# Optimization experiments

Hardware: AMD Instinct MI355X
Metric: run time of the kernel (lower is better)

The kernel has to match this reference:

```python
import jax, jax.numpy as jnp
import numpy as np

B, S, N = 65536, 512, 514
EPS = 1e-16


def setup_inputs() -> dict:
    key = jax.random.key(0)
    kx, kv = jax.random.split(key)
    x = jax.random.normal(kx, (B, S), dtype=jnp.float32)
    # parameters: uniform(-1,1) then normalized along the size dim (as in reset_parameters)
    v = jax.random.uniform(kv, (N, S, 1), dtype=jnp.float32, minval=-1.0, maxval=1.0)
    v = v / jnp.linalg.norm(v, axis=1, keepdims=True)
    return {"x": x, "vectors": v}


def _calculate_Q(vectors):
    # vectors: [N, S, 1]
    Nv, Sv, _ = vectors.shape
    v = vectors[..., 0]                                   # [N, S]
    inner = jnp.sum(v * v, axis=1)[:, None, None]         # [N, 1, 1]  (v^T v)
    outer = v[:, :, None] * v[:, None, :]                 # [N, S, S]  (v v^T)
    I = jnp.eye(Sv, dtype=vectors.dtype)
    mats = I[None, :, :] - 2.0 * outer / (inner + EPS)    # [N, S, S]

    def step(Q, M):
        return Q @ M, None

    Q, _ = jax.lax.scan(step, mats[0], mats[1:])          # sequential product M0 @ M1 @ ... @ M_{N-1}
    return Q


def reference(x, vectors):
    Q = _calculate_Q(vectors)
    return x @ Q.T
```

## Files before the change

### kernel.cpp

```cpp
#include <hip/hip_runtime.h>


#define LDG 520
#define GROWS 528
#define LDU 520
#define NHH 514
#define SDIM 512
#define EPS_HH 1e-16f
#define EPLD 132

typedef float f32x4 __attribute__((ext_vector_type(4)));
typedef __fp16 h16x2 __attribute__((ext_vector_type(2)));
typedef __fp16 h16x8 __attribute__((ext_vector_type(8)));

__device__ __forceinline__ void gl_lds16(const void* g, void* l) {
  __builtin_amdgcn_global_load_lds((const __attribute__((address_space(1))) void*)g,
                                   (__attribute__((address_space(3))) void*)l, 16, 0, 0);
}

__global__ __launch_bounds__(256) void gram_k(const float* __restrict__ v,
                                              float* __restrict__ G) {
  __shared__ float As[32][36];
  __shared__ float Bs[32][36];
  const int t = threadIdx.x;
  const int i0 = blockIdx.y * 32, j0 = blockIdx.x * 32;
  const int tx = t & 15, ty = t >> 4;
  const int r = t >> 3, c4 = (t & 7) * 4;
  float acc00 = 0.f, acc01 = 0.f, acc10 = 0.f, acc11 = 0.f;
  for (int kb = 0; kb < SDIM; kb += 32) {
    __syncthreads();
    float4 av = (i0 + r < NHH)
                    ? *(const float4*)(v + (size_t)(i0 + r) * SDIM + kb + c4)
                    : make_float4(0.f, 0.f, 0.f, 0.f);
    float4 bv = (j0 + r < NHH)
                    ? *(const float4*)(v + (size_t)(j0 + r) * SDIM + kb + c4)
                    : make_float4(0.f, 0.f, 0.f, 0.f);
    *(float4*)&As[r][c4] = av;
    *(float4*)&Bs[r][c4] = bv;
    __syncthreads();
#pragma unroll
    for (int kk = 0; kk < 32; kk++) {
      float a0 = As[ty * 2][kk], a1 = As[ty * 2 + 1][kk];
      float b0 = Bs[tx * 2][kk], b1 = Bs[tx * 2 + 1][kk];
      acc00 = fmaf(a0, b0, acc00);
      acc01 = fmaf(a0, b1, acc01);
      acc10 = fmaf(a1, b0, acc10);
      acc11 = fmaf(a1, b1, acc11);
    }
  }
  int row0 = i0 + ty * 2, col0 = j0 + tx * 2;
  if (row0 < NHH) {
    if (col0 < LDG) G[(size_t)row0 * LDG + col0] = acc00;
    if (col0 + 1 < LDG) G[(size_t)row0 * LDG + col0 + 1] = acc01;
  }
  if (row0 + 1 < NHH) {
    if (col0 < LDG) G[(size_t)(row0 + 1) * LDG + col0] = acc10;
    if (col0 + 1 < LDG) G[(size_t)(row0 + 1) * LDG + col0 + 1] = acc11;
  }
}

__global__ __launch_bounds__(256, 1) void solve_k(const float* __restrict__ v,
                                                  const float* __restrict__ G,
                                                  float* __restrict__ U) {
  const int lane = threadIdx.x & 63;
  const int s = blockIdx.x * 4 + (threadIdx.x >> 6);
  float W[9];
  float binv[9];
#pragma unroll
  for (int k = 0; k < 9; k++) {
    int j = k * 64 + lane;
    W[k] = (j < NHH) ? v[(size_t)j * SDIM + s] : 0.f;
    binv[k] = (j < NHH) ? (2.0f / (G[(size_t)j * LDG + j] + EPS_HH)) : 0.f;
  }
  float* Urow = U + (size_t)s * LDU;
  float g[8][9];
#pragma unroll
  for (int p = 0; p < 7; p++) {
    const float* gp = G + (size_t)p * LDG + lane;
#pragma unroll
    for (int k = 0; k < 9; k++) g[p][k] = gp[k * 64];
  }
  float usave = 0.f;

#define HH_STEP(I, CI, SLOT, PSLOT, DO_PF)                                 \
  do {                                                                     \
    const int i_ = (I);                                                    \
    if (DO_PF) {                                                           \
      const float* gp_ = G + (size_t)(i_ + 7) * LDG + lane;                \
      _Pragma("unroll") for (int k = 0; k < 9; k++) g[PSLOT][k] =          \
          gp_[k * 64];                                                     \
    }                                                                      \
    const int sl_ = i_ & 63;                                               \
    float u_ = __shfl(W[CI] * binv[CI], sl_, 64);                          \
    if (lane == sl_) usave = u_;                                           \
    _Pragma("unroll") for (int k = 0; k < 9; k++) W[k] =                   \
        fmaf(-u_, g[SLOT][k], W[k]);                                       \
    if (sl_ == 63) Urow[i_ - 63 + lane] = usave;                           \
  } while (0)

#pragma unroll
  for (int c = 0; c < 8; c++) {
    for (int q = 0; q < 8; q++) {
      const int base = c * 64 + q * 8;
      HH_STEP(base + 0, c, 0, 7, true);
      HH_STEP(base + 1, c, 1, 0, true);
      HH_STEP(base + 2, c, 2, 1, true);
      HH_STEP(base + 3, c, 3, 2, true);
      HH_STEP(base + 4, c, 4, 3, true);
      HH_STEP(base + 5, c, 5, 4, true);
      HH_STEP(base + 6, c, 6, 5, true);
      HH_STEP(base + 7, c, 7, 6, true);
    }
  }
  HH_STEP(512, 8, 0, 0, false);
  HH_STEP(513, 8, 1, 0, false);
  if (lane < 2) Urow[512 + lane] = usave;
#undef HH_STEP
}

__global__ __launch_bounds__(256) void qtt_k(const float* __restrict__ v,
                                             const float* __restrict__ U,
                                             __fp16* __restrict__ QTT) {
  __shared__ float As[32][36];
  __shared__ float Bs[32][36];
  const int t = threadIdx.x;
  const int s0 = blockIdx.y * 32, t0 = blockIdx.x * 32;
  const int tx = t & 15, ty = t >> 4;
  const int r = t >> 3, c4 = (t & 7) * 4;
  float acc00 = 0.f, acc01 = 0.f, acc10 = 0.f, acc11 = 0.f;
  for (int kb = 0; kb < NHH; kb += 32) {
    __syncthreads();
    float4 av = *(const float4*)(U + (size_t)(s0 + r) * LDU + kb + c4);
    float4 bv = (kb + r < NHH)
                    ? *(const float4*)(v + (size_t)(kb + r) * SDIM + t0 + c4)
                    : make_float4(0.f, 0.f, 0.f, 0.f);
    *(float4*)&As[r][c4] = av;
    *(float4*)&Bs[r][c4] = bv;
    __syncthreads();
#pragma unroll
    for (int kk = 0; kk < 32; kk++) {
      float a0 = As[ty * 2][kk], a1 = As[ty * 2 + 1][kk];
      float b0 = Bs[kk][tx * 2], b1 = Bs[kk][tx * 2 + 1];
      acc00 = fmaf(a0, b0, acc00);
      acc01 = fmaf(a0, b1, acc01);
      acc10 = fmaf(a1, b0, acc10);
      acc11 = fmaf(a1, b1, acc11);
    }
  }
  int row0 = s0 + ty * 2, col0 = t0 + tx * 2;
  QTT[(size_t)row0 * SDIM + col0] =
      (__fp16)(((row0 == col0) ? 1.f : 0.f) - acc00);
  QTT[(size_t)row0 * SDIM + col0 + 1] =
      (__fp16)(((row0 == col0 + 1) ? 1.f : 0.f) - acc01);
  QTT[(size_t)(row0 + 1) * SDIM + col0] =
      (__fp16)(((row0 + 1 == col0) ? 1.f : 0.f) - acc10);
  QTT[(size_t)(row0 + 1) * SDIM + col0 + 1] =
      (__fp16)(((row0 + 1 == col0 + 1) ? 1.f : 0.f) - acc11);
}

__global__ __launch_bounds__(256) void gemm_k(const float* __restrict__ X,
                                              const __fp16* __restrict__ BT,
                                              float* __restrict__ C) {
  __shared__ __attribute__((aligned(16))) float As[2][128 * 32];
  __shared__ __attribute__((aligned(16))) __fp16 Bs[2][128 * 32];
  const int t = threadIdx.x;
  const int lane = t & 63, wave = t >> 6;
  const int bid = blockIdx.x;
  const int xcd = bid & 7;
  const int g = bid >> 3;
  const int m0 = ((g >> 2) * 8 + xcd) * 128;
  const int n0 = (g & 3) * 128;
  const int wm = (wave >> 1) * 64, wn = (wave & 1) * 64;
  const int rr = lane & 15, kg = lane >> 4;
  const int wb = t & ~63;

  f32x4 acc[4][4];
#pragma unroll
  for (int a = 0; a < 4; a++)
#pragma unroll
    for (int b = 0; b < 4; b++) acc[a][b] = (f32x4){0.f, 0.f, 0.f, 0.f};

  auto STAGE = [&](int k0, int buf) {
#pragma unroll
    for (int q = 0; q < 4; q++) {
      int idx = q * 256 + t;
      int r = idx >> 3, u = idx & 7;
      int c = (u ^ (r & 7)) * 4;
      const float* gp = X + (size_t)(m0 + r) * 512 + k0 + c;
      gl_lds16(gp, (void*)&As[buf][(size_t)(q * 256 + wb) * 4]);
    }
#pragma unroll
    for (int q = 0; q < 2; q++) {
      int idx = q * 256 + t;
      int r = idx >> 2, u = idx & 3;
      int c = (u ^ (r & 3)) * 8;
      const __fp16* gp = BT + (size_t)(n0 + r) * 512 + k0 + c;
      gl_lds16(gp, (void*)&Bs[buf][(size_t)(q * 256 + wb) * 8]);
    }
  };

  STAGE(0, 0);

  const int swzA = rr & 7;
  const int swzB = rr & 3;

  for (int ks = 0; ks < 16; ++ks) {
    const int cur = ks & 1;
    if (ks < 15) {
      STAGE((ks + 1) * 32, cur ^ 1);
      asm volatile("s_waitcnt vmcnt(6)" ::: "memory");
    } else {
      asm volatile("s_waitcnt vmcnt(0)" ::: "memory");
    }
    asm volatile("s_barrier" ::: "memory");

    h16x8 af[4], bf[4];
#pragma unroll
    for (int mi = 0; mi < 4; mi++) {
      const float* rowp = &As[cur][(size_t)(wm + mi * 16 + rr) * 32];
      float4 lo = *(const float4*)(rowp + (size_t)((2 * kg + 0) ^ swzA) * 4);
      float4 hi = *(const float4*)(rowp + (size_t)((2 * kg + 1) ^ swzA) * 4);
      h16x2 p0 = __builtin_amdgcn_cvt_pkrtz(lo.x, lo.y);
      h16x2 p1 = __builtin_amdgcn_cvt_pkrtz(lo.z, lo.w);
      h16x2 p2 = __builtin_amdgcn_cvt_pkrtz(hi.x, hi.y);
      h16x2 p3 = __builtin_amdgcn_cvt_pkrtz(hi.z, hi.w);
      h16x8 a = {p0[0], p0[1], p1[0], p1[1], p2[0], p2[1], p3[0], p3[1]};
      af[mi] = a;
    }
#pragma unroll
    for (int ni = 0; ni < 4; ni++) {
      const __fp16* rowp = &Bs[cur][(size_t)(wn + ni * 16 + rr) * 32];
      bf[ni] = *(const h16x8*)(rowp + (size_t)(kg ^ swzB) * 8);
    }

#pragma unroll
    for (int mi = 0; mi < 4; mi++)
#pragma unroll
      for (int ni = 0; ni < 4; ni++)
        acc[mi][ni] =
            __builtin_amdgcn_mfma_f32_16x16x32_f16(af[mi], bf[ni], acc[mi][ni], 0, 0, 0);

    asm volatile("s_barrier" ::: "memory");
  }

  float* Ep = (float*)As;
  const int lr = (lane >> 4) * 4;
  const int lc = wn + rr;
  const int buf = wave >> 1;
#pragma unroll
  for (int rnd = 0; rnd < 4; rnd++) {
    float* bp = Ep + buf * (16 * EPLD);
#pragma unroll
    for (int ni = 0; ni < 4; ni++)
#pragma unroll
      for (int q = 0; q < 4; q++)
        bp[(lr + q) * EPLD + lc + ni * 16] = acc[rnd][ni][q];
    __syncthreads();
#pragma unroll
    for (int j = 0; j < 4; j++) {
      int fidx = j * 256 + t;
      int b = fidx >> 9;
      int wi = fidx & 511;
      int lrow = wi >> 5;
      int c4 = wi & 31;
      int grow = m0 + b * 64 + rnd * 16 + lrow;
      *(float4*)(C + (size_t)grow * 512 + n0 + c4 * 4) =
          *(const float4*)(Ep + b * (16 * EPLD) + lrow * EPLD + c4 * 4);
    }
    __syncthreads();
  }
}

extern "C" void kernel_launch(void* const* d_in, const int* in_sizes, int n_in,
                              void* d_out, int out_size, void* d_ws, size_t ws_size,
                              hipStream_t stream) {
  const float* x = (const float*)d_in[0];
  const float* v = (const float*)d_in[1];
  float* out = (float*)d_out;

  char* w = (char*)d_ws;
  float* G = (float*)w;
  float* U = (float*)(w + (size_t)GROWS * LDG * 4);
  __fp16* QTT =
      (__fp16*)(w + (size_t)GROWS * LDG * 4 + (size_t)512 * LDU * 4);

  gram_k<<<dim3(17, 17), 256, 0, stream>>>(v, G);
  solve_k<<<128, 256, 0, stream>>>(v, G, U);
  qtt_k<<<dim3(16, 16), 256, 0, stream>>>(v, U, QTT);
  gemm_k<<<2048, 256, 0, stream>>>(x, QTT, out);
}
```

Baseline: 361.7 us.

## Enlarge gram/qtt tiles to 4x4 per thread and spread solve across more blocks

The gram and QTT matrix kernels move from 32x32 tiles with 2x2 outputs per thread to 64x64 tiles with 4x4 outputs per thread. K-major LDS layout allows float4 fragment reads, raising arithmetic intensity per LDS access and cutting the launched block count. The solve kernel now runs 2 waves per block across 256 blocks to spread rows over more CUs, and uses readlane instead of a shuffle for the broadcast. The QTT kernel pads K to 528 with clamped, zeroed loads and writes packed fp16x4 stores. Larger tiles give fewer blocks (81 and 64), which may underfill the GPU on these small matrices.

```diff
diff --git a/kernel.cpp b/kernel.cpp
--- a/kernel.cpp
+++ b/kernel.cpp
@@ -11,6 +11,7 @@
 
 typedef float f32x4 __attribute__((ext_vector_type(4)));
 typedef __fp16 h16x2 __attribute__((ext_vector_type(2)));
+typedef __fp16 h16x4v __attribute__((ext_vector_type(4)));
 typedef __fp16 h16x8 __attribute__((ext_vector_type(8)));
 
 __device__ __forceinline__ void gl_lds16(const void* g, void* l) {
@@ -20,50 +21,64 @@
 
 __global__ __launch_bounds__(256) void gram_k(const float* __restrict__ v,
                                               float* __restrict__ G) {
-  __shared__ float As[32][36];
-  __shared__ float Bs[32][36];
+  __shared__ float As[16][68];
+  __shared__ float Bs[16][68];
   const int t = threadIdx.x;
-  const int i0 = blockIdx.y * 32, j0 = blockIdx.x * 32;
+  const int i0 = blockIdx.y * 64, j0 = blockIdx.x * 64;
   const int tx = t & 15, ty = t >> 4;
-  const int r = t >> 3, c4 = (t & 7) * 4;
-  float acc00 = 0.f, acc01 = 0.f, acc10 = 0.f, acc11 = 0.f;
-  for (int kb = 0; kb < SDIM; kb += 32) {
-    __syncthreads();
-    float4 av = (i0 + r < NHH)
-                    ? *(const float4*)(v + (size_t)(i0 + r) * SDIM + kb + c4)
+  const int lr = t & 63, lk = (t >> 6) * 4;
+  float acc[4][4];
+#pragma unroll
+  for (int a = 0; a < 4; a++)
+#pragma unroll
+    for (int b = 0; b < 4; b++) acc[a][b] = 0.f;
+
+  for (int kb = 0; kb < SDIM; kb += 16) {
+    __syncthreads();
+    float4 av = (i0 + lr < NHH)
+                    ? *(const float4*)(v + (size_t)(i0 + lr) * SDIM + kb + lk)
                     : make_float4(0.f, 0.f, 0.f, 0.f);
-    float4 bv = (j0 + r < NHH)
-                    ? *(const float4*)(v + (size_t)(j0 + r) * SDIM + kb + c4)
+    float4 bv = (j0 + lr < NHH)
+                    ? *(const float4*)(v + (size_t)(j0 + lr) * SDIM + kb + lk)
                     : make_float4(0.f, 0.f, 0.f, 0.f);
-    *(float4*)&As[r][c4] = av;
-    *(float4*)&Bs[r][c4] = bv;
-    __syncthreads();
-#pragma unroll
-    for (int kk = 0; kk < 32; kk++) {
-      float a0 = As[ty * 2][kk], a1 = As[ty * 2 + 1][kk];
-      float b0 = Bs[tx * 2][kk], b1 = Bs[tx * 2 + 1][kk];
-      acc00 = fmaf(a0, b0, acc00);
-      acc01 = fmaf(a0, b1, acc01);
-      acc10 = fmaf(a1, b0, acc10);
-      acc11 = fmaf(a1, b1, acc11);
-    }
-  }
-  int row0 = i0 + ty * 2, col0 = j0 + tx * 2;
-  if (row0 < NHH) {
-    if (col0 < LDG) G[(size_t)row0 * LDG + col0] = acc00;
-    if (col0 + 1 < LDG) G[(size_t)row0 * LDG + col0 + 1] = acc01;
-  }
-  if (row0 + 1 < NHH) {
-    if (col0 < LDG) G[(size_t)(row0 + 1) * LDG + col0] = acc10;
-    if (col0 + 1 < LDG) G[(size_t)(row0 + 1) * LDG + col0 + 1] = acc11;
-  }
-}
-
-__global__ __launch_bounds__(256, 1) void solve_k(const float* __restrict__ v,
+    As[lk + 0][lr] = av.x;
+    As[lk + 1][lr] = av.y;
+    As[lk + 2][lr] = av.z;
+    As[lk + 3][lr] = av.w;
+    Bs[lk + 0][lr] = bv.x;
+    Bs[lk + 1][lr] = bv.y;
+    Bs[lk + 2][lr] = bv.z;
+    Bs[lk + 3][lr] = bv.w;
+    __syncthreads();
+#pragma unroll
+    for (int kk = 0; kk < 16; kk++) {
+      float4 a4 = *(const float4*)&As[kk][ty * 4];
+      float4 b4 = *(const float4*)&Bs[kk][tx * 4];
+      float aa[4] = {a4.x, a4.y, a4.z, a4.w};
+      float bb[4] = {b4.x, b4.y, b4.z, b4.w};
+#pragma unroll
+      for (int a = 0; a < 4; a++)
+#pragma unroll
+        for (int b = 0; b < 4; b++) acc[a][b] = fmaf(aa[a], bb[b], acc[a][b]);
+    }
+  }
+#pragma unroll
+  for (int a = 0; a < 4; a++) {
+    int row = i0 + ty * 4 + a;
+    if (row >= NHH) continue;
+#pragma unroll
+    for (int b = 0; b < 4; b++) {
+      int col = j0 + tx * 4 + b;
+      if (col < LDG) G[(size_t)row * LDG + col] = acc[a][b];
+    }
+  }
+}
+
+__global__ __launch_bounds__(128, 1) void solve_k(const float* __restrict__ v,
                                                   const float* __restrict__ G,
                                                   float* __restrict__ U) {
   const int lane = threadIdx.x & 63;
-  const int s = blockIdx.x * 4 + (threadIdx.x >> 6);
+  const int s = blockIdx.x * 2 + (threadIdx.x >> 6);
   float W[9];
   float binv[9];
 #pragma unroll
@@ -91,7 +106,9 @@
           gp_[k * 64];                                                     \
     }                                                                      \
     const int sl_ = i_ & 63;                                               \
-    float u_ = __shfl(W[CI] * binv[CI], sl_, 64);                          \
+    float u_ = __builtin_bit_cast(                                         \
+        float, __builtin_amdgcn_readlane(                                  \
+                   __builtin_bit_cast(int, W[CI] * binv[CI]), sl_));       \
     if (lane == sl_) usave = u_;                                           \
     _Pragma("unroll") for (int k = 0; k < 9; k++) W[k] =                   \
         fmaf(-u_, g[SLOT][k], W[k]);                                       \
@@ -121,41 +138,60 @@
 __global__ __launch_bounds__(256) void qtt_k(const float* __restrict__ v,
                                              const float* __restrict__ U,
                                              __fp16* __restrict__ QTT) {
-  __shared__ float As[32][36];
-  __shared__ float Bs[32][36];
+  __shared__ float As[16][68];
+  __shared__ float Bs[16][68];
   const int t = threadIdx.x;
-  const int s0 = blockIdx.y * 32, t0 = blockIdx.x * 32;
+  const int s0 = blockIdx.y * 64, t0 = blockIdx.x * 64;
   const int tx = t & 15, ty = t >> 4;
-  const int r = t >> 3, c4 = (t & 7) * 4;
-  float acc00 = 0.f, acc01 = 0.f, acc10 = 0.f, acc11 = 0.f;
-  for (int kb = 0; kb < NHH; kb += 32) {
-    __syncthreads();
-    float4 av = *(const float4*)(U + (size_t)(s0 + r) * LDU + kb + c4);
-    float4 bv = (kb + r < NHH)
-                    ? *(const float4*)(v + (size_t)(kb + r) * SDIM + t0 + c4)
+  const int lr = t & 63, lk = (t >> 6) * 4;
+  const int brow = t >> 4, bc4 = (t & 15) * 4;
+  float acc[4][4];
+#pragma unroll
+  for (int a = 0; a < 4; a++)
+#pragma unroll
+    for (int b = 0; b < 4; b++) acc[a][b] = 0.f;
+
+  for (int kb = 0; kb < 528; kb += 16) {
+    __syncthreads();
+    int cl = kb + lk;
+    if (cl > 516) cl = 516;
+    float4 av = *(const float4*)(U + (size_t)(s0 + lr) * LDU + cl);
+    if (kb + lk + 0 >= NHH) av.x = 0.f;
+    if (kb + lk + 1 >= NHH) av.y = 0.f;
+    if (kb + lk + 2 >= NHH) av.z = 0.f;
+    if (kb + lk + 3 >= NHH) av.w = 0.f;
+    float4 bv = (kb + brow < NHH)
+                    ? *(const float4*)(v + (size_t)(kb + brow) * SDIM + t0 + bc4)
                     : make_float4(0.f, 0.f, 0.f, 0.f);
-    *(float4*)&As[r][c4] = av;
-    *(float4*)&Bs[r][c4] = bv;
-    __syncthreads();
-#pragma unroll
-    for (int kk = 0; kk < 32; kk++) {
-      float a0 = As[ty * 2][kk], a1 = As[ty * 2 + 1][kk];
-      float b0 = Bs[kk][tx * 2], b1 = Bs[kk][tx * 2 + 1];
-      acc00 = fmaf(a0, b0, acc00);
-      acc01 = fmaf(a0, b1, acc01);
-      acc10 = fmaf(a1, b0, acc10);
-      acc11 = fmaf(a1, b1, acc11);
-    }
-  }
-  int row0 = s0 + ty * 2, col0 = t0 + tx * 2;
-  QTT[(size_t)row0 * SDIM + col0] =
-      (__fp16)(((row0 == col0) ? 1.f : 0.f) - acc00);
-  QTT[(size_t)row0 * SDIM + col0 + 1] =
-      (__fp16)(((row0 == col0 + 1) ? 1.f : 0.f) - acc01);
-  QTT[(size_t)(row0 + 1) * SDIM + col0] =
-      (__fp16)(((row0 + 1 == col0) ? 1.f : 0.f) - acc10);
-  QTT[(size_t)(row0 + 1) * SDIM + col0 + 1] =
-      (__fp16)(((row0 + 1 == col0 + 1) ? 1.f : 0.f) - acc11);
+    As[lk + 0][lr] = av.x;
+    As[lk + 1][lr] = av.y;
+    As[lk + 2][lr] = av.z;
+    As[lk + 3][lr] = av.w;
+    *(float4*)&Bs[brow][bc4] = bv;
+    __syncthreads();
+#pragma unroll
+    for (int kk = 0; kk < 16; kk++) {
+      float4 a4 = *(const float4*)&As[kk][ty * 4];
+      float4 b4 = *(const float4*)&Bs[kk][tx * 4];
+      float aa[4] = {a4.x, a4.y, a4.z, a4.w};
+      float bb[4] = {b4.x, b4.y, b4.z, b4.w};
+#pragma unroll
+      for (int a = 0; a < 4; a++)
+#pragma unroll
+        for (int b = 0; b < 4; b++) acc[a][b] = fmaf(aa[a], bb[b], acc[a][b]);
+    }
+  }
+#pragma unroll
+  for (int a = 0; a < 4; a++) {
+    int row = s0 + ty * 4 + a;
+    h16x4v o;
+#pragma unroll
+    for (int b = 0; b < 4; b++) {
+      int col = t0 + tx * 4 + b;
+      o[b] = (__fp16)(((row == col) ? 1.f : 0.f) - acc[a][b]);
+    }
+    *(h16x4v*)(QTT + (size_t)row * SDIM + t0 + tx * 4) = o;
+  }
 }
 
 __global__ __launch_bounds__(256) void gemm_k(const float* __restrict__ X,
@@ -284,8 +320,8 @@
   __fp16* QTT =
       (__fp16*)(w + (size_t)GROWS * LDG * 4 + (size_t)512 * LDU * 4);
 
-  gram_k<<<dim3(17, 17), 256, 0, stream>>>(v, G);
-  solve_k<<<128, 256, 0, stream>>>(v, G, U);
-  qtt_k<<<dim3(16, 16), 256, 0, stream>>>(v, U, QTT);
+  gram_k<<<dim3(9, 9), 256, 0, stream>>>(v, G);
+  solve_k<<<256, 128, 0, stream>>>(v, G, U);
+  qtt_k<<<dim3(8, 8), 256, 0, stream>>>(v, U, QTT);
   gemm_k<<<2048, 256, 0, stream>>>(x, QTT, out);
 }
```

Measured after the change: 379.9 us. 5.0% more time.
